# Optimization experiments

Hardware: AMD Instinct MI355X
Metric: run time of the kernel (lower is better)

## Reference

```python
import jax, jax.numpy as jnp
import numpy as np

TAU = 2.0        # LIF membrane time constant
VTH = 1.0        # firing threshold
ALPHA = 4.0      # surrogate sigmoid sharpness
BN_EPS = 1e-5

@jax.custom_vjp
def heaviside_surrogate(x):
    # Forward: hard threshold. Backward: sigmoid surrogate gradient (alpha=4).
    return (x >= 0.0).astype(x.dtype)

def _hs_fwd(x):
    return heaviside_surrogate(x), x

def _hs_bwd(x, g):
    s = jax.nn.sigmoid(ALPHA * x)
    return (g * ALPHA * s * (1.0 - s),)

heaviside_surrogate.defvjp(_hs_fwd, _hs_bwd)


def setup_inputs() -> dict:
    key = jax.random.key(0)
    k1, k2 = jax.random.split(key)
    B, Cin, T, Cout = 64, 512, 1024, 256
    x = jax.random.normal(k1, (B, Cin, T), dtype=jnp.float32)
    W = jax.random.normal(k2, (Cout, Cin), dtype=jnp.float32) * (1.0 / np.sqrt(Cin))
    gamma = jnp.ones((Cout,), dtype=jnp.float32)
    beta = jnp.zeros((Cout,), dtype=jnp.float32)
    run_mean = jnp.zeros((Cout,), dtype=jnp.float32)
    run_var = jnp.ones((Cout,), dtype=jnp.float32)
    return {"x": x, "W": W, "gamma": gamma, "beta": beta,
            "run_mean": run_mean, "run_var": run_var}


def reference(x, W, gamma, beta, run_mean, run_var):
    # Dropout is identity in eval mode.
    # conv1d, kernel_size=1, no bias -> pointwise GEMM over channels: [B,Cin,T] -> [B,Cout,T]
    y = jnp.einsum('bct,oc->bot', x, W)
    # BatchNorm1d (inference, running stats), per-channel affine
    inv = jax.lax.rsqrt(run_var + BN_EPS)
    y = (y - run_mean[None, :, None]) * (inv * gamma)[None, :, None] + beta[None, :, None]
    # LIF recurrence over the time dim (last axis), hard reset to 0, detach_reset.
    yt = jnp.transpose(y, (2, 0, 1))  # [T, B, Cout]

    def step(v, x_t):
        v = v + (x_t - v) / TAU              # decay_input charge
        s = heaviside_surrogate(v - VTH)     # spike via surrogate threshold
        v = v * (1.0 - jax.lax.stop_gradient(s))  # hard reset (detached)
        return v, s

    v0 = jnp.zeros(yt.shape[1:], dtype=yt.dtype)
    _, spikes = jax.lax.scan(step, v0, yt)   # spikes: [T, B, Cout]
    # out.mean(dim=-1) == spike rate over time
    return spikes.mean(axis=0)               # [B, Cout]
```

## Files before the change

kernel.cpp:

```cpp
#include <hip/hip_runtime.h>
#include <math.h>

typedef _Float16 f16;
typedef __attribute__((ext_vector_type(8)))  _Float16 f16v8;
typedef __attribute__((ext_vector_type(4)))  __fp16   h16v4;
typedef __attribute__((ext_vector_type(16))) float    f32x16;
typedef __attribute__((ext_vector_type(4)))  float    f32x4;

namespace {
constexpr int kB = 64, kCin = 512, kT = 1024, kCout = 256;
constexpr size_t kYBytes     = (size_t)kB * kT * kCout * 4;
constexpr size_t kWfragBytes = (size_t)32 * 8 * 2 * 64 * 16;
constexpr size_t kSBytes     = kCout * 4;
constexpr size_t kWsNeed     = kYBytes + kWfragBytes + kSBytes;
}

__global__ void wsplit16_kernel(const float* __restrict__ W, const float* __restrict__ gamma,
                                const float* __restrict__ rvar,
                                f16* __restrict__ wfrag, float* __restrict__ sarr) {
    const int kc = blockIdx.x, osub = blockIdx.y, p = blockIdx.z;
    const int lane = threadIdx.x;
    const int o  = osub * 32 + (lane & 31);
    const int kb = kc * 16 + (lane >> 5) * 8;
    f16v8 frag;
#pragma unroll
    for (int j = 0; j < 8; ++j) {
        const float w = 32.0f * W[o * kCin + kb + j];
        const f16 h = (f16)w;
        const float r = w - (float)h;
        const f16 l = (f16)(r * 2048.0f);
        frag[j] = p ? l : h;
    }
    *reinterpret_cast<f16v8*>(wfrag + ((size_t)((kc * 8 + osub) * 2 + p) * 64 + lane) * 8) = frag;
    if (kc == 0 && osub == 0 && p == 0) {
#pragma unroll
        for (int j = 0; j < 4; ++j) {
            const int oo = j * 64 + lane;
            sarr[oo] = (float)((double)gamma[oo] / sqrt((double)rvar[oo] + 1e-5));
        }
    }
}

__global__ __launch_bounds__(256, 2)
void gemm_f16_kernel(const float* __restrict__ x, const f16* __restrict__ wfrag,
                     const float* __restrict__ sarr, const float* __restrict__ rmean,
                     const float* __restrict__ beta, float* __restrict__ y) {
    __shared__ union {
        unsigned int Bd[2][64 * 20];
        float        tb[4][32 * 36];
    } sh;

    const int tid  = threadIdx.x;
    const int lane = tid & 63;
    const int wave = tid >> 6;
    const int n = lane & 31, q = lane >> 5;
    const int b   = blockIdx.y;
    const int tg0 = blockIdx.x * 64;
    const float* __restrict__ xb = x + ((size_t)b << 19);
    const f16v8* __restrict__ wf = reinterpret_cast<const f16v8*>(wfrag);

    const int st_t = tid & 63;
    const int kpp  = wave;
    const int st_sw = (st_t >> 3) & 3;
    const int wr_base = 20 * st_t + 2 * (kpp & 1);
    const int s0 = ((0 + (kpp >> 1)) ^ st_sw) * 4;
    const int s1 = ((2 + (kpp >> 1)) ^ st_sw) * 4;

    f32x16 accA[2][2] = {};
    f32x16 accB[2][2] = {};
    f16v8  af[2][2][2];
    float  xq[4][4];

    auto loadX = [&](int kc, float (&xd)[4]) {
        const float* px = xb + (size_t)(kc * 16 + 4 * kpp) * kT + tg0 + st_t;
#pragma unroll
        for (int r = 0; r < 4; ++r) xd[r] = px[(size_t)r * kT];
    };
    auto loadA = [&](int kc, f16v8 (&ad)[2][2]) {
#pragma unroll
        for (int i = 0; i < 2; ++i)
#pragma unroll
            for (int p = 0; p < 2; ++p)
                ad[i][p] = wf[(size_t)((kc * 8 + wave * 2 + i) * 2 + p) * 64 + lane];
    };
    auto stage = [&](int buf, const float (&xd)[4]) {
        auto h01 = __builtin_amdgcn_cvt_pkrtz(xd[0], xd[1]);
        auto h23 = __builtin_amdgcn_cvt_pkrtz(xd[2], xd[3]);
        auto l01 = __builtin_amdgcn_cvt_pkrtz((xd[0] - (float)h01[0]) * 2048.0f,
                                              (xd[1] - (float)h01[1]) * 2048.0f);
        auto l23 = __builtin_amdgcn_cvt_pkrtz((xd[2] - (float)h23[0]) * 2048.0f,
                                              (xd[3] - (float)h23[1]) * 2048.0f);
        h16v4 hv, lv;
        hv[0] = h01[0]; hv[1] = h01[1]; hv[2] = h23[0]; hv[3] = h23[1];
        lv[0] = l01[0]; lv[1] = l01[1]; lv[2] = l23[0]; lv[3] = l23[1];
        *reinterpret_cast<h16v4*>(&sh.Bd[buf][wr_base + s0]) = hv;
        *reinterpret_cast<h16v4*>(&sh.Bd[buf][wr_base + s1]) = lv;
    };
    auto domfma = [&](int buf, const f16v8 (&ad)[2][2]) {
#pragma unroll
        for (int s = 0; s < 2; ++s) {
            const int t = s * 32 + n;
            const int sw = (t >> 3) & 3;
            const f16v8 bh = *reinterpret_cast<const f16v8*>(&sh.Bd[buf][20 * t + 4 * ((0 + q) ^ sw)]);
            const f16v8 bl = *reinterpret_cast<const f16v8*>(&sh.Bd[buf][20 * t + 4 * ((2 + q) ^ sw)]);
#pragma unroll
            for (int i = 0; i < 2; ++i) {
                accA[i][s] = __builtin_amdgcn_mfma_f32_32x32x16_f16(ad[i][0], bh, accA[i][s], 0, 0, 0);
                accB[i][s] = __builtin_amdgcn_mfma_f32_32x32x16_f16(ad[i][0], bl, accB[i][s], 0, 0, 0);
                accB[i][s] = __builtin_amdgcn_mfma_f32_32x32x16_f16(ad[i][1], bh, accB[i][s], 0, 0, 0);
            }
        }
    };

    loadX(0, xq[0]); loadX(1, xq[1]); loadX(2, xq[2]); loadX(3, xq[3]);
    loadA(0, af[0]);
    stage(0, xq[0]);
    asm volatile("s_waitcnt lgkmcnt(0)\n\ts_barrier" ::: "memory");

    for (int kc4 = 0; kc4 < 8; ++kc4) {
#pragma unroll
        for (int u = 0; u < 4; ++u) {
            const int kc = kc4 * 4 + u;
            const int cur = kc & 1, nxt = cur ^ 1;
            if (kc < 31) loadA(kc + 1, af[nxt]);
            if (kc < 31) stage(nxt, xq[(u + 1) & 3]);
            if (kc < 28) loadX(kc + 4, xq[u]);
            domfma(cur, af[cur]);
            asm volatile("s_waitcnt lgkmcnt(0)\n\ts_barrier" ::: "memory");
        }
    }

    float* tb = sh.tb[wave];
#pragma unroll
    for (int i = 0; i < 2; ++i)
#pragma unroll
        for (int s = 0; s < 2; ++s) {
            const f32x16 v = accA[i][s] + accB[i][s] * 4.8828125e-4f;
            asm volatile("s_waitcnt lgkmcnt(0)" ::: "memory");
#pragma unroll
            for (int g = 0; g < 4; ++g) {
                f32x4 t4;
                t4.x = v[4 * g + 0]; t4.y = v[4 * g + 1];
                t4.z = v[4 * g + 2]; t4.w = v[4 * g + 3];
                *reinterpret_cast<f32x4*>(tb + n * 36 + g * 8 + q * 4) = t4;
            }
            asm volatile("s_waitcnt lgkmcnt(0)" ::: "memory");
#pragma unroll
            for (int r4 = 0; r4 < 4; ++r4) {
                const int fidx = lane + 64 * r4;
                const int tl = fidx >> 3, o4 = fidx & 7;
                const int og = wave * 64 + i * 32 + o4 * 4;
                f32x4 val = *reinterpret_cast<const f32x4*>(tb + tl * 36 + o4 * 4);
                const f32x4 sv = *reinterpret_cast<const f32x4*>(sarr + og);
                const f32x4 mv = *reinterpret_cast<const f32x4*>(rmean + og);
                const f32x4 bv = *reinterpret_cast<const f32x4*>(beta + og);
                val = (val * 0.03125f - mv) * sv + bv;
                const size_t t = (size_t)tg0 + s * 32 + tl;
                *reinterpret_cast<f32x4*>(y + ((((size_t)b << 10) + t) << 8) + og) = val;
            }
        }
}

__global__ __launch_bounds__(64)
void lif_kernel(const float* __restrict__ y, float* __restrict__ out) {
    const int b = blockIdx.x >> 2;
    const int o = ((blockIdx.x & 3) << 6) + threadIdx.x;
    const float* __restrict__ yb = y + ((size_t)b << 18);
    float v = 0.f;
    int cnt = 0;
    float buf[4][32];
    auto loadb = [&](int i, float (&bf)[32]) {
#pragma unroll
        for (int j = 0; j < 32; ++j)
            bf[j] = yb[(size_t)(i * 32 + j) * 256 + o];
    };
    auto stepb = [&](const float (&bf)[32]) {
#pragma unroll
        for (int j = 0; j < 32; ++j) {
            v = v + (bf[j] - v) * 0.5f;
            if (v - 1.0f >= 0.0f) { ++cnt; v = 0.f; }
        }
    };
    loadb(0, buf[0]); loadb(1, buf[1]); loadb(2, buf[2]);
    for (int i4 = 0; i4 < 8; ++i4) {
#pragma unroll
        for (int u = 0; u < 4; ++u) {
            const int i = i4 * 4 + u;
            if (i < 29) loadb(i + 3, buf[(u + 3) & 3]);
            stepb(buf[u]);
        }
    }
    out[((size_t)b << 8) + o] = (float)cnt * (1.0f / 1024.0f);
}

namespace fb {
constexpr int kOTile = 32, kTTile = 128, kCc = 64;
constexpr int kNtt = kT / kTTile, kNcc = kCin / kCc, kYPad = 132;
}

__global__ void wt_transpose_kernel(const float* __restrict__ W, float* __restrict__ Wt) {
    int idx = blockIdx.x * 256 + threadIdx.x;
    int c = idx >> 8, o = idx & 255;
    Wt[idx] = W[o * kCin + c];
}

__global__ __launch_bounds__(256, 2)
void snn_fused_kernel(const float* __restrict__ x, const float* __restrict__ Wt,
                      const float* __restrict__ gamma, const float* __restrict__ beta,
                      const float* __restrict__ rmean, const float* __restrict__ rvar,
                      float* __restrict__ out) {
    using namespace fb;
    __shared__ float xs[kCc][kTTile];
    __shared__ float ws[kCc][kOTile];
    __shared__ float ytile[kOTile][kYPad];
    __shared__ float sarr[kOTile], barr[kOTile], marr[kOTile], vstate[kOTile];
    __shared__ int scnt[kOTile];
    const int tid = threadIdx.x, tx = tid & 31, ty = tid >> 5;
    const int b = blockIdx.y, o_blk = blockIdx.x * kOTile;
    if (tid < kOTile) {
        const int o = o_blk + tid;
        const double dinv = 1.0 / sqrt((double)rvar[o] + 1e-5);
        sarr[tid] = (float)(dinv * (double)gamma[o]);
        barr[tid] = beta[o]; marr[tid] = rmean[o];
        vstate[tid] = 0.0f; scnt[tid] = 0;
    }
    __syncthreads();
    const float* xb = x + (size_t)b * kCin * kT;
    for (int tt = 0; tt < kNtt; ++tt) {
        float acc[4][4];
#pragma unroll
        for (int i = 0; i < 4; ++i)
#pragma unroll
            for (int j = 0; j < 4; ++j) acc[i][j] = 0.0f;
        const int t0 = tt * kTTile;
        for (int cc = 0; cc < kNcc; ++cc) {
#pragma unroll
            for (int k = 0; k < 8; ++k) {
                const int f = tid + 256 * k;
                const int c = f >> 5, tq = f & 31;
                *reinterpret_cast<float4*>(&xs[c][tq * 4]) = *reinterpret_cast<const float4*>(
                    xb + (size_t)(cc * kCc + c) * kT + t0 + tq * 4);
            }
#pragma unroll
            for (int k = 0; k < 2; ++k) {
                const int f = tid + 256 * k;
                const int c = f >> 3, oq = f & 7;
                *reinterpret_cast<float4*>(&ws[c][oq * 4]) = *reinterpret_cast<const float4*>(
                    Wt + (size_t)(cc * kCc + c) * kCout + o_blk + oq * 4);
            }
            __syncthreads();
#pragma unroll 8
            for (int c = 0; c < kCc; ++c) {
                const float4 xv = *reinterpret_cast<const float4*>(&xs[c][tx * 4]);
                const float4 wv = *reinterpret_cast<const float4*>(&ws[c][ty * 4]);
                const float xf[4] = {xv.x, xv.y, xv.z, xv.w};
                const float wf4[4] = {wv.x, wv.y, wv.z, wv.w};
#pragma unroll
                for (int i = 0; i < 4; ++i)
#pragma unroll
                    for (int j = 0; j < 4; ++j) acc[i][j] += wf4[i] * xf[j];
            }
            __syncthreads();
        }
#pragma unroll
        for (int i = 0; i < 4; ++i) {
            const int o = ty * 4 + i;
            const float s = sarr[o], bb2 = barr[o], m = marr[o];
#pragma unroll
            for (int j = 0; j < 4; ++j) ytile[o][tx * 4 + j] = (acc[i][j] - m) * s + bb2;
        }
        __syncthreads();
        if (tid < kOTile) {
            float vv = vstate[tid];
            int cnt = 0;
#pragma unroll 4
            for (int t = 0; t < kTTile; ++t) {
                const float yv = ytile[tid][t];
                vv = vv + (yv - vv) * 0.5f;
                if (vv - 1.0f >= 0.0f) { cnt++; vv = 0.0f; }
            }
            vstate[tid] = vv; scnt[tid] += cnt;
        }
        __syncthreads();
    }
    if (tid < kOTile) out[b * kCout + o_blk + tid] = (float)scnt[tid] * (1.0f / 1024.0f);
}

extern "C" void kernel_launch(void* const* d_in, const int* in_sizes, int n_in,
                              void* d_out, int out_size, void* d_ws, size_t ws_size,
                              hipStream_t stream) {
    const float* x     = (const float*)d_in[0];
    const float* W     = (const float*)d_in[1];
    const float* gamma = (const float*)d_in[2];
    const float* beta  = (const float*)d_in[3];
    const float* rmean = (const float*)d_in[4];
    const float* rvar  = (const float*)d_in[5];
    float* out = (float*)d_out;

    if (ws_size >= kWsNeed) {
        float* y     = (float*)d_ws;
        f16*   wfrag = (f16*)((char*)d_ws + kYBytes);
        float* sarr  = (float*)((char*)d_ws + kYBytes + kWfragBytes);
        wsplit16_kernel<<<dim3(32, 8, 2), 64, 0, stream>>>(W, gamma, rvar, wfrag, sarr);
        gemm_f16_kernel<<<dim3(16, 64), 256, 0, stream>>>(x, wfrag, sarr, rmean, beta, y);
        lif_kernel<<<256, 64, 0, stream>>>(y, out);
    } else {
        float* Wt = (float*)d_ws;
        wt_transpose_kernel<<<(kCin * kCout) / 256, 256, 0, stream>>>(W, Wt);
        snn_fused_kernel<<<dim3(kCout / fb::kOTile, kB), 256, 0, stream>>>(
            x, Wt, gamma, beta, rmean, rvar, out);
    }
}
```

Measured before the change: 252.8 us.

## Store GEMM output time-contiguous, quad-buffer B staging, vectorize LIF reads

The intermediate y is now written as [B, Cout, T] straight from the MFMA accumulators, dropping the LDS transpose epilogue. The LIF kernel can then read each neuron's time series as contiguous float4 loads instead of strided per-timestep loads. The GEMM main loop moves to four LDS buffers with a barrier every two k-chunks and raises wave priority around the MFMA block, to cut sync overhead. The cost is scattered 4-byte global stores in the GEMM epilogue, where consecutive lanes write along t, plus more LDS per block.

```diff
diff --git a/kernel.cpp b/kernel.cpp
--- a/kernel.cpp
+++ b/kernel.cpp
@@ -44,11 +44,8 @@
 __global__ __launch_bounds__(256, 2)
 void gemm_f16_kernel(const float* __restrict__ x, const f16* __restrict__ wfrag,
                      const float* __restrict__ sarr, const float* __restrict__ rmean,
-                     const float* __restrict__ beta, float* __restrict__ y) {
-    __shared__ union {
-        unsigned int Bd[2][64 * 20];
-        float        tb[4][32 * 36];
-    } sh;
+                     const float* __restrict__ beta, float* __restrict__ yt) {
+    __shared__ unsigned int Bd[4][64 * 20];
 
     const int tid  = threadIdx.x;
     const int lane = tid & 63;
@@ -93,16 +90,17 @@
         h16v4 hv, lv;
         hv[0] = h01[0]; hv[1] = h01[1]; hv[2] = h23[0]; hv[3] = h23[1];
         lv[0] = l01[0]; lv[1] = l01[1]; lv[2] = l23[0]; lv[3] = l23[1];
-        *reinterpret_cast<h16v4*>(&sh.Bd[buf][wr_base + s0]) = hv;
-        *reinterpret_cast<h16v4*>(&sh.Bd[buf][wr_base + s1]) = lv;
+        *reinterpret_cast<h16v4*>(&Bd[buf][wr_base + s0]) = hv;
+        *reinterpret_cast<h16v4*>(&Bd[buf][wr_base + s1]) = lv;
     };
     auto domfma = [&](int buf, const f16v8 (&ad)[2][2]) {
+        __builtin_amdgcn_s_setprio(1);
 #pragma unroll
         for (int s = 0; s < 2; ++s) {
             const int t = s * 32 + n;
             const int sw = (t >> 3) & 3;
-            const f16v8 bh = *reinterpret_cast<const f16v8*>(&sh.Bd[buf][20 * t + 4 * ((0 + q) ^ sw)]);
-            const f16v8 bl = *reinterpret_cast<const f16v8*>(&sh.Bd[buf][20 * t + 4 * ((2 + q) ^ sw)]);
+            const f16v8 bh = *reinterpret_cast<const f16v8*>(&Bd[buf][20 * t + 4 * ((0 + q) ^ sw)]);
+            const f16v8 bl = *reinterpret_cast<const f16v8*>(&Bd[buf][20 * t + 4 * ((2 + q) ^ sw)]);
 #pragma unroll
             for (int i = 0; i < 2; ++i) {
                 accA[i][s] = __builtin_amdgcn_mfma_f32_32x32x16_f16(ad[i][0], bh, accA[i][s], 0, 0, 0);
@@ -110,84 +108,84 @@
                 accB[i][s] = __builtin_amdgcn_mfma_f32_32x32x16_f16(ad[i][1], bh, accB[i][s], 0, 0, 0);
             }
         }
+        __builtin_amdgcn_s_setprio(0);
     };
 
     loadX(0, xq[0]); loadX(1, xq[1]); loadX(2, xq[2]); loadX(3, xq[3]);
     loadA(0, af[0]);
     stage(0, xq[0]);
+    stage(1, xq[1]);
     asm volatile("s_waitcnt lgkmcnt(0)\n\ts_barrier" ::: "memory");
 
     for (int kc4 = 0; kc4 < 8; ++kc4) {
 #pragma unroll
         for (int u = 0; u < 4; ++u) {
             const int kc = kc4 * 4 + u;
-            const int cur = kc & 1, nxt = cur ^ 1;
-            if (kc < 31) loadA(kc + 1, af[nxt]);
-            if (kc < 31) stage(nxt, xq[(u + 1) & 3]);
+            if (kc < 31) loadA(kc + 1, af[(u + 1) & 1]);
+            if (kc < 30) stage((u + 2) & 3, xq[(u + 2) & 3]);
             if (kc < 28) loadX(kc + 4, xq[u]);
-            domfma(cur, af[cur]);
-            asm volatile("s_waitcnt lgkmcnt(0)\n\ts_barrier" ::: "memory");
-        }
-    }
-
-    float* tb = sh.tb[wave];
-#pragma unroll
-    for (int i = 0; i < 2; ++i)
+            domfma(u, af[u & 1]);
+            if (u & 1)
+                asm volatile("s_waitcnt lgkmcnt(0)\n\ts_barrier" ::: "memory");
+        }
+    }
+
+#pragma unroll
+    for (int i = 0; i < 2; ++i) {
+        f32x4 sv[4], mv[4], bv[4];
+#pragma unroll
+        for (int g = 0; g < 4; ++g) {
+            const int og = wave * 64 + i * 32 + g * 8 + q * 4;
+            sv[g] = *reinterpret_cast<const f32x4*>(sarr + og);
+            mv[g] = *reinterpret_cast<const f32x4*>(rmean + og);
+            bv[g] = *reinterpret_cast<const f32x4*>(beta + og);
+        }
 #pragma unroll
         for (int s = 0; s < 2; ++s) {
             const f32x16 v = accA[i][s] + accB[i][s] * 4.8828125e-4f;
-            asm volatile("s_waitcnt lgkmcnt(0)" ::: "memory");
-#pragma unroll
-            for (int g = 0; g < 4; ++g) {
-                f32x4 t4;
-                t4.x = v[4 * g + 0]; t4.y = v[4 * g + 1];
-                t4.z = v[4 * g + 2]; t4.w = v[4 * g + 3];
-                *reinterpret_cast<f32x4*>(tb + n * 36 + g * 8 + q * 4) = t4;
-            }
-            asm volatile("s_waitcnt lgkmcnt(0)" ::: "memory");
-#pragma unroll
-            for (int r4 = 0; r4 < 4; ++r4) {
-                const int fidx = lane + 64 * r4;
-                const int tl = fidx >> 3, o4 = fidx & 7;
-                const int og = wave * 64 + i * 32 + o4 * 4;
-                f32x4 val = *reinterpret_cast<const f32x4*>(tb + tl * 36 + o4 * 4);
-                const f32x4 sv = *reinterpret_cast<const f32x4*>(sarr + og);
-                const f32x4 mv = *reinterpret_cast<const f32x4*>(rmean + og);
-                const f32x4 bv = *reinterpret_cast<const f32x4*>(beta + og);
-                val = (val * 0.03125f - mv) * sv + bv;
-                const size_t t = (size_t)tg0 + s * 32 + tl;
-                *reinterpret_cast<f32x4*>(y + ((((size_t)b << 10) + t) << 8) + og) = val;
-            }
-        }
+            const size_t t = (size_t)tg0 + s * 32 + n;
+#pragma unroll
+            for (int g = 0; g < 4; ++g)
+#pragma unroll
+                for (int r2 = 0; r2 < 4; ++r2) {
+                    const int o = wave * 64 + i * 32 + g * 8 + q * 4 + r2;
+                    const float val = (v[4 * g + r2] * 0.03125f - mv[g][r2]) * sv[g][r2] + bv[g][r2];
+                    yt[(((size_t)b << 8) + (size_t)o) * 1024 + t] = val;
+                }
+        }
+    }
 }
 
 __global__ __launch_bounds__(64)
-void lif_kernel(const float* __restrict__ y, float* __restrict__ out) {
+void lif_kernel(const float* __restrict__ yt, float* __restrict__ out) {
     const int b = blockIdx.x >> 2;
     const int o = ((blockIdx.x & 3) << 6) + threadIdx.x;
-    const float* __restrict__ yb = y + ((size_t)b << 18);
+    const f32x4* __restrict__ row =
+        reinterpret_cast<const f32x4*>(yt) + (((size_t)b << 8) + (size_t)o) * 256;
     float v = 0.f;
     int cnt = 0;
-    float buf[4][32];
-    auto loadb = [&](int i, float (&bf)[32]) {
-#pragma unroll
-        for (int j = 0; j < 32; ++j)
-            bf[j] = yb[(size_t)(i * 32 + j) * 256 + o];
-    };
-    auto stepb = [&](const float (&bf)[32]) {
-#pragma unroll
-        for (int j = 0; j < 32; ++j) {
-            v = v + (bf[j] - v) * 0.5f;
+    f32x4 qb[16];
+#pragma unroll
+    for (int u = 0; u < 16; ++u) qb[u] = row[u];
+    for (int jj = 0; jj < 15; ++jj) {
+#pragma unroll
+        for (int u = 0; u < 16; ++u) {
+            const f32x4 cv = qb[u];
+            qb[u] = row[jj * 16 + u + 16];
+#pragma unroll
+            for (int e = 0; e < 4; ++e) {
+                v = v + (cv[e] - v) * 0.5f;
+                if (v - 1.0f >= 0.0f) { ++cnt; v = 0.f; }
+            }
+        }
+    }
+#pragma unroll
+    for (int u = 0; u < 16; ++u) {
+        const f32x4 cv = qb[u];
+#pragma unroll
+        for (int e = 0; e < 4; ++e) {
+            v = v + (cv[e] - v) * 0.5f;
             if (v - 1.0f >= 0.0f) { ++cnt; v = 0.f; }
-        }
-    };
-    loadb(0, buf[0]); loadb(1, buf[1]); loadb(2, buf[2]);
-    for (int i4 = 0; i4 < 8; ++i4) {
-#pragma unroll
-        for (int u = 0; u < 4; ++u) {
-            const int i = i4 * 4 + u;
-            if (i < 29) loadb(i + 3, buf[(u + 3) & 3]);
-            stepb(buf[u]);
         }
     }
     out[((size_t)b << 8) + o] = (float)cnt * (1.0f / 1024.0f);
@@ -298,12 +296,12 @@
     float* out = (float*)d_out;
 
     if (ws_size >= kWsNeed) {
-        float* y     = (float*)d_ws;
+        float* yt    = (float*)d_ws;
         f16*   wfrag = (f16*)((char*)d_ws + kYBytes);
         float* sarr  = (float*)((char*)d_ws + kYBytes + kWfragBytes);
         wsplit16_kernel<<<dim3(32, 8, 2), 64, 0, stream>>>(W, gamma, rvar, wfrag, sarr);
-        gemm_f16_kernel<<<dim3(16, 64), 256, 0, stream>>>(x, wfrag, sarr, rmean, beta, y);
-        lif_kernel<<<256, 64, 0, stream>>>(y, out);
+        gemm_f16_kernel<<<dim3(16, 64), 256, 0, stream>>>(x, wfrag, sarr, rmean, beta, yt);
+        lif_kernel<<<256, 64, 0, stream>>>(yt, out);
     } else {
         float* Wt = (float*)d_ws;
         wt_transpose_kernel<<<(kCin * kCout) / 256, 256, 0, stream>>>(W, Wt);
```

Result: no change. 255.9 us (+1.3%).
